# Kernel tuning notes

Hardware: AMD Instinct MI355X
Metric: run time of the kernel (lower is better)

## Reference

```python
import jax, jax.numpy as jnp
import numpy as np

NEG_INF = float('-inf')

def setup_inputs() -> dict:
    key = jax.random.key(0)
    k1, k2, k3, k4 = jax.random.split(key, 4)
    B, H, S, D = 2, 16, 2048, 64
    query = jax.random.normal(k1, (B, H, S, D), dtype=jnp.float32)
    k_ = jax.random.normal(k2, (B, H, S, D), dtype=jnp.float32)
    v_ = jax.random.normal(k3, (B, H, S, D), dtype=jnp.float32)
    attn_mask = jax.random.randint(k4, (B, S, S), 0, 2).astype(bool)
    # ensure diagonal is unmasked so every causal row has >=1 valid key
    diag = jnp.arange(S)
    attn_mask = attn_mask.at[:, diag, diag].set(True)
    return {"query": query, "key": k_, "value": v_, "attn_mask": attn_mask}

def reference(query, key, value, attn_mask):
    # query/key/value: [B, H, S, D]; attn_mask: [B, S, S] bool, True = keep
    B, H, S, D = query.shape
    scale = D ** (-0.5)
    scores = jnp.einsum('bhqd,bhkd->bhqk', query, key) * scale
    # custom mask (True = keep)
    scores = jnp.where(attn_mask[:, None, :, :], scores, NEG_INF)
    # causal mask: disallow j > i
    causal = jnp.triu(jnp.ones((S, S), dtype=bool), k=1)  # True above diagonal
    scores = jnp.where(causal[None, None, :, :], NEG_INF, scores)
    probs = jax.nn.softmax(scores, axis=-1)
    # dropout omitted (eval mode / deterministic reference)
    out = jnp.einsum('bhqk,bhkd->bhqd', probs, value)
    return out
```

## Files before the change

### kernel.cpp

```cpp
#include <hip/hip_runtime.h>
#include <hip/hip_bf16.h>

#define NS 2048
#define ND 64

typedef __attribute__((ext_vector_type(8))) short short8;
typedef __attribute__((ext_vector_type(4))) short short4v;
typedef __attribute__((ext_vector_type(4))) float f32x4;

static __device__ __forceinline__ short f2bf(float f) {
    union { __hip_bfloat16 h; short s; } u;
    u.h = __float2bfloat16(f);
    return u.s;
}
static __device__ __forceinline__ unsigned int pack2(float lo, float hi) {
    return (unsigned int)(unsigned short)f2bf(lo) |
           ((unsigned int)(unsigned short)f2bf(hi) << 16);
}
static __device__ __forceinline__ float exp2_fast(float x) {
    float r;
    asm("v_exp_f32 %0, %1" : "=v"(r) : "v"(x));
    return r;
}
static __device__ __forceinline__ unsigned int cvt_pk_bf16(float lo, float hi) {
    unsigned int w;
    asm("v_cvt_pk_bf16_f32 %0, %1, %2" : "=v"(w) : "v"(lo), "v"(hi));
    return w;
}

__global__ void detect_mask_kernel(const unsigned char* __restrict__ mask,
                                   int* __restrict__ flag) {
    const int i = threadIdx.x;
    unsigned int acc = 0;
    const uchar4* p = (const uchar4*)(mask + i * 64);
    #pragma unroll
    for (int j = 0; j < 16; ++j) {
        uchar4 v = p[j];
        acc |= (unsigned int)v.y | v.z | v.w;
    }
    const unsigned long long any = __ballot(acc != 0);
    if (i == 0) *flag = (any == 0ULL) ? 4 : 1;
}

__global__ void prep_all(const float* __restrict__ K,
                         const float* __restrict__ V,
                         const unsigned char* __restrict__ M,
                         const int* __restrict__ flag,
                         unsigned char* __restrict__ IMG,
                         unsigned int* __restrict__ Mbits) {
    if (blockIdx.x < 2048) {
        const int bid = blockIdx.x;
        const int bh = bid >> 6, T = bid & 63;
        const int i = threadIdx.x;
        __shared__ __align__(16) unsigned char img[8192];

        const int row = i >> 3;
        const int d0  = (i & 7) * 8;

        {
            const float* src = K + ((size_t)(bh * NS + T * 32 + row)) * ND + d0;
            float4 f0 = ((const float4*)src)[0];
            float4 f1 = ((const float4*)src)[1];
            const float f[8] = {f0.x, f0.y, f0.z, f0.w, f1.x, f1.y, f1.z, f1.w};
            const int n = row >> 4, cc = row & 15;
            #pragma unroll
            for (int jp = 0; jp < 4; ++jp) {
                const int d  = d0 + 2 * jp;
                const int ch = d >> 5, dd = d & 31;
                const int g  = (dd & 15) >> 2;
                const int jj = (dd >> 4) * 2 + ((dd >> 1) & 1);
                *(unsigned int*)(img + (n * 2 + ch) * 1024 + (g * 16 + cc) * 16 + jj * 4) =
                    pack2(f[2 * jp], f[2 * jp + 1]);
            }
        }
        {
            const int kv = row;
            const float* src = V + ((size_t)(bh * NS + T * 32 + kv)) * ND + d0;
            float4 f0 = ((const float4*)src)[0];
            float4 f1 = ((const float4*)src)[1];
            const float f[8] = {f0.x, f0.y, f0.z, f0.w, f1.x, f1.y, f1.z, f1.w};
            const int kl  = kv & ~1;
            const int q15 = kl & 15;
            const int g   = q15 >> 2;
            const int jj  = (kl >> 4) * 2 + ((q15 >> 1) & 1);
            const int half = (kv & 1) * 2;
            #pragma unroll
            for (int e = 0; e < 8; ++e) {
                const int d  = d0 + e;
                const int n4 = d >> 4, cv = d & 15;
                *(short*)(img + 4096 + n4 * 1024 + (g * 16 + cv) * 16 + jj * 4 + half) =
                    f2bf(f[e]);
            }
        }
        __syncthreads();
        uint4* dst = (uint4*)(IMG + ((size_t)bid << 13));
        const uint4* srcl = (const uint4*)img;
        dst[i * 2]     = srcl[i * 2];
        dst[i * 2 + 1] = srcl[i * 2 + 1];
    } else {
        const int id3 = (blockIdx.x - 2048) * 256 + threadIdx.x;
        const int tt = id3 & 63, q = (id3 >> 6) & 2047, b = id3 >> 17;
        const int ms = *flag;
        unsigned int w = 0;
        if (ms == 1) {
            const uint4* p = (const uint4*)(M + ((size_t)(b * NS + q)) * NS + tt * 32);
            uint4 A = p[0], B = p[1];
            const unsigned int u[8] = {A.x, A.y, A.z, A.w, B.x, B.y, B.z, B.w};
            #pragma unroll
            for (int i = 0; i < 8; ++i) {
                const unsigned int nib = (((u[i] & 0x01010101u) * 0x01020408u) >> 24) & 0xFu;
                w |= nib << (4 * i);
            }
        } else {
            const uint4* p = (const uint4*)(M + (((size_t)(b * NS + q)) * NS) * 4 + tt * 128);
            #pragma unroll
            for (int i = 0; i < 8; ++i) {
                uint4 A = p[i];
                w |= ((A.x & 1u) << (4 * i)) | ((A.y & 1u) << (4 * i + 1)) |
                     ((A.z & 1u) << (4 * i + 2)) | ((A.w & 1u) << (4 * i + 3));
            }
        }
        const int qrel = q - 32 * tt;
        if (qrel < 0) w = 0;
        else if (qrel < 31) w &= ((2u << qrel) - 1u);
        Mbits[((size_t)(b * 64 + (q >> 5)) * 64 + tt) * 32 + (q & 31)] = w;
    }
}

#define GLD(gsrc, ldst) __builtin_amdgcn_global_load_lds( \
    (const __attribute__((address_space(1))) unsigned int*)(gsrc), \
    (__attribute__((address_space(3))) unsigned int*)(ldst), 16, 0, 0)

__launch_bounds__(256, 4)
__global__ void attn_main(const float* __restrict__ Q,
                          const unsigned char* __restrict__ IMG,
                          const unsigned int* __restrict__ Mbits,
                          float* __restrict__ O) {
    const int idx = blockIdx.x;
    const int j   = (idx & 511) >> 5;
    const int bh  = idx & 31;
    const int qi  = (idx < 512) ? (31 - j) : j;
    const int b   = bh >> 4;

    const int tid  = threadIdx.x;
    const int wid  = tid >> 6;
    const int lane = tid & 63;
    const int g = lane >> 4;
    const int c = lane & 15;
    const int p = wid & 1;
    const int s = wid >> 1;

    const int q0w = qi * 64 + s * 32;

    const size_t bhoff = (size_t)bh * NS * ND;
    const float* Qb = Q + bhoff;
    float*       Ob = O + bhoff;
    const unsigned char* Tb = IMG + ((size_t)bh << 19);
    const unsigned int*  Mw = Mbits + ((size_t)(b * 64 + 2 * qi + s) << 11);

    __shared__ __align__(16) unsigned char smem[2][16384];

    const float QS = 0.18033688f;
    short8 aq[2][2];
    #pragma unroll
    for (int m = 0; m < 2; ++m) {
        const float* qrow = Qb + (size_t)(q0w + m * 16 + c) * ND;
        #pragma unroll
        for (int ch = 0; ch < 2; ++ch) {
            float4 x0 = *reinterpret_cast<const float4*>(qrow + ch * 32 + g * 4);
            float4 x1 = *reinterpret_cast<const float4*>(qrow + ch * 32 + 16 + g * 4);
            short8 fr;
            fr[0]=f2bf(x0.x*QS); fr[1]=f2bf(x0.y*QS); fr[2]=f2bf(x0.z*QS); fr[3]=f2bf(x0.w*QS);
            fr[4]=f2bf(x1.x*QS); fr[5]=f2bf(x1.y*QS); fr[6]=f2bf(x1.z*QS); fr[7]=f2bf(x1.w*QS);
            aq[m][ch] = fr;
        }
    }

    const short ov = (c == 0) ? (short)0x3F80 : (short)0;
    short8 onesf;
    #pragma unroll
    for (int e = 0; e < 8; ++e) onesf[e] = ov;

    f32x4 acc[2][4];
    f32x4 acc_l[2];
    #pragma unroll
    for (int m = 0; m < 2; ++m) {
        acc_l[m] = (f32x4){0.f, 0.f, 0.f, 0.f};
        #pragma unroll
        for (int n4 = 0; n4 < 4; ++n4) acc[m][n4] = (f32x4){0.f, 0.f, 0.f, 0.f};
    }

    const int NP   = qi + 1;
    const int tmax = 2 * qi + s;

#define STAGE(B, TP) do { \
    const unsigned char* gp_ = Tb + ((size_t)(2 * (TP)) << 13) + (wid << 10) + (lane << 4); \
    unsigned char* lb_ = &smem[B][wid << 10]; \
    GLD(gp_,         lb_); \
    GLD(gp_ +  4096, lb_ +  4096); \
    GLD(gp_ +  8192, lb_ +  8192); \
    GLD(gp_ + 12288, lb_ + 12288); \
} while (0)

    STAGE(0, 0);
    unsigned int mk0 = Mw[p * 32 + c];
    unsigned int mk1 = Mw[p * 32 + 16 + c];
    asm volatile("s_waitcnt vmcnt(0)" ::: "memory");
    __syncthreads();

    for (int tp = 0; tp < NP; ++tp) {
        const int cur = tp & 1;
        const int t = 2 * tp + p;
        const bool havenext = (tp + 1 < NP);
        unsigned int nk0 = 0, nk1 = 0;
        if (havenext) {
            STAGE(cur ^ 1, tp + 1);
            nk0 = Mw[(t + 2) * 32 + c];
            nk1 = Mw[(t + 2) * 32 + 16 + c];
        }

        if (t <= tmax) {
            const unsigned char* kb = smem[cur] + (p << 13);
            const unsigned char* vb = kb + 4096;

            short8 kf[4], av[4];
            #pragma unroll
            for (int k4 = 0; k4 < 4; ++k4)
                kf[k4] = *(const short8*)(kb + k4 * 1024 + (lane << 4));
            #pragma unroll
            for (int n4 = 0; n4 < 4; ++n4)
                av[n4] = *(const short8*)(vb + n4 * 1024 + (lane << 4));

            #pragma unroll
            for (int m = 0; m < 2; ++m) {
                f32x4 s0 = (f32x4){0.f, 0.f, 0.f, 0.f};
                f32x4 s1 = (f32x4){0.f, 0.f, 0.f, 0.f};
                s0 = __builtin_amdgcn_mfma_f32_16x16x32_bf16(kf[0], aq[m][0], s0, 0, 0, 0);
                s0 = __builtin_amdgcn_mfma_f32_16x16x32_bf16(kf[1], aq[m][1], s0, 0, 0, 0);
                s1 = __builtin_amdgcn_mfma_f32_16x16x32_bf16(kf[2], aq[m][0], s1, 0, 0, 0);
                s1 = __builtin_amdgcn_mfma_f32_16x16x32_bf16(kf[3], aq[m][1], s1, 0, 0, 0);

                const unsigned int mk = m ? mk1 : mk0;

                float pv[8];
                #pragma unroll
                for (int r = 0; r < 4; ++r) {
                    const unsigned int b0 = (mk >> (4 * g + r)) & 1u;
                    const unsigned int b1 = (mk >> (16 + 4 * g + r)) & 1u;
                    pv[r]     = exp2_fast(b0 ? s0[r] : -INFINITY);
                    pv[4 + r] = exp2_fast(b1 ? s1[r] : -INFINITY);
                }
                union { unsigned int u[4]; short8 v; } pfu;
                pfu.u[0] = cvt_pk_bf16(pv[0], pv[1]);
                pfu.u[1] = cvt_pk_bf16(pv[2], pv[3]);
                pfu.u[2] = cvt_pk_bf16(pv[4], pv[5]);
                pfu.u[3] = cvt_pk_bf16(pv[6], pv[7]);
                const short8 pf = pfu.v;

                #pragma unroll
                for (int n4 = 0; n4 < 4; ++n4)
                    acc[m][n4] = __builtin_amdgcn_mfma_f32_16x16x32_bf16(av[n4], pf, acc[m][n4], 0, 0, 0);
                acc_l[m] = __builtin_amdgcn_mfma_f32_16x16x32_bf16(onesf, pf, acc_l[m], 0, 0, 0);
            }
        }

        mk0 = nk0; mk1 = nk1;
        asm volatile("s_waitcnt vmcnt(0)" ::: "memory");
        __syncthreads();
    }

    float* MB = (float*)smem;
    __syncthreads();
    if (p == 1) {
        #pragma unroll
        for (int m = 0; m < 2; ++m) {
            #pragma unroll
            for (int n4 = 0; n4 < 4; ++n4)
                *(f32x4*)&MB[(((s * 2 + m) * 4 + n4) * 64 + lane) * 4] = acc[m][n4];
            *(f32x4*)&MB[4096 + ((s * 2 + m) * 64 + lane) * 4] = acc_l[m];
        }
    }
    __syncthreads();
    if (p == 0) {
        #pragma unroll
        for (int m = 0; m < 2; ++m) {
            #pragma unroll
            for (int n4 = 0; n4 < 4; ++n4) {
                f32x4 o = *(const f32x4*)&MB[(((s * 2 + m) * 4 + n4) * 64 + lane) * 4];
                acc[m][n4][0] += o[0]; acc[m][n4][1] += o[1];
                acc[m][n4][2] += o[2]; acc[m][n4][3] += o[3];
            }
            f32x4 ol = *(const f32x4*)&MB[4096 + ((s * 2 + m) * 64 + lane) * 4];
            acc_l[m][0] += ol[0];
        }
        #pragma unroll
        for (int m = 0; m < 2; ++m) {
            const int q = q0w + m * 16 + c;
            const float lsum = __shfl(acc_l[m][0], c);
            const float inv = (lsum > 0.f) ? (1.f / lsum) : 0.f;
            float* orow = Ob + (size_t)q * ND;
            #pragma unroll
            for (int n4 = 0; n4 < 4; ++n4) {
                float4 o;
                o.x = acc[m][n4][0] * inv;
                o.y = acc[m][n4][1] * inv;
                o.z = acc[m][n4][2] * inv;
                o.w = acc[m][n4][3] * inv;
                *(float4*)(orow + n4 * 16 + 4 * g) = o;
            }
        }
    }
#undef STAGE
}

__launch_bounds__(128, 2)
__global__ void attn_fwd_fb(const float* __restrict__ Q,
                            const float* __restrict__ K,
                            const float* __restrict__ V,
                            const unsigned char* __restrict__ M,
                            float* __restrict__ O,
                            const int* __restrict__ mstride_p) {
    const int ms  = *mstride_p;
    const int idx = blockIdx.x;
    const int qi  = 31 - (idx >> 5);
    const int bh  = idx & 31;
    const int b   = bh >> 4;

    const int tid  = threadIdx.x;
    const int wid  = tid >> 6;
    const int lane = tid & 63;
    const int g = lane >> 4;
    const int c = lane & 15;

    const int q0w = qi * 64 + wid * 32;

    const size_t bhoff = (size_t)bh * NS * ND;
    const float* Qb = Q + bhoff;
    const float* Kb = K + bhoff;
    const float* Vb = V + bhoff;
    float*       Ob = O + bhoff;
    const unsigned char* Mb = M + (size_t)b * NS * NS * (size_t)ms;

    __shared__ __align__(16) unsigned char smem[2][8192];

    short8 aq[2][2];
    #pragma unroll
    for (int m = 0; m < 2; ++m) {
        const float* qrow = Qb + (size_t)(q0w + m * 16 + c) * ND;
        #pragma unroll
        for (int ch = 0; ch < 2; ++ch) {
            float4 x0 = *reinterpret_cast<const float4*>(qrow + ch * 32 + g * 4);
            float4 x1 = *reinterpret_cast<const float4*>(qrow + ch * 32 + 16 + g * 4);
            short8 fr;
            fr[0]=f2bf(x0.x); fr[1]=f2bf(x0.y); fr[2]=f2bf(x0.z); fr[3]=f2bf(x0.w);
            fr[4]=f2bf(x1.x); fr[5]=f2bf(x1.y); fr[6]=f2bf(x1.z); fr[7]=f2bf(x1.w);
            aq[m][ch] = fr;
        }
    }

    f32x4 acc[2][4];
    float m_run[2], l_run[2];
    #pragma unroll
    for (int m = 0; m < 2; ++m) {
        m_run[m] = -INFINITY; l_run[m] = 0.f;
        #pragma unroll
        for (int n4 = 0; n4 < 4; ++n4) acc[m][n4] = (f32x4){0.f, 0.f, 0.f, 0.f};
    }

    const int NT = 2 * qi + 2;

    const int krow = tid >> 2;
    const int kcb  = (tid & 3) * 16;
    const int ksw  = (krow & 7) << 4;
    const int vkp  = tid >> 3;
    const int vdb  = tid & 7;
    const int vg   = (vkp >> 1) & 3;
    const int vep  = (vkp & 1) + 2 * (vkp >> 3);
    const float* kbase = Kb + (size_t)krow * ND + kcb;
    const float* vbase = Vb + (size_t)(2 * vkp) * ND + vdb * 8;

    float4 kin0, kin1, kin2, kin3, vin0, vin1, vin2, vin3;

#define STAGE_LOAD(T) do { \
    const float* kp_ = kbase + (size_t)(T) * 32 * ND; \
    kin0 = *(const float4*)(kp_);      kin1 = *(const float4*)(kp_ + 4); \
    kin2 = *(const float4*)(kp_ + 8);  kin3 = *(const float4*)(kp_ + 12); \
    const float* vp_ = vbase + (size_t)(T) * 32 * ND; \
    vin0 = *(const float4*)(vp_);      vin1 = *(const float4*)(vp_ + 4); \
    vin2 = *(const float4*)(vp_ + ND); vin3 = *(const float4*)(vp_ + ND + 4); \
} while (0)

#define STAGE_WRITE(BUF) do { \
    unsigned char* kb_ = smem[BUF]; \
    short8 w0, w1; \
    w0[0]=f2bf(kin0.x); w0[1]=f2bf(kin0.y); w0[2]=f2bf(kin0.z); w0[3]=f2bf(kin0.w); \
    w0[4]=f2bf(kin1.x); w0[5]=f2bf(kin1.y); w0[6]=f2bf(kin1.z); w0[7]=f2bf(kin1.w); \
    w1[0]=f2bf(kin2.x); w1[1]=f2bf(kin2.y); w1[2]=f2bf(kin2.z); w1[3]=f2bf(kin2.w); \
    w1[4]=f2bf(kin3.x); w1[5]=f2bf(kin3.y); w1[6]=f2bf(kin3.z); w1[7]=f2bf(kin3.w); \
    *(short8*)(kb_ + krow * 128 + ((kcb * 2) ^ ksw))      = w0; \
    *(short8*)(kb_ + krow * 128 + ((kcb * 2 + 16) ^ ksw)) = w1; \
    unsigned char* vb_ = smem[BUF] + 4096; \
    const float lo_[8] = {vin0.x, vin0.y, vin0.z, vin0.w, vin1.x, vin1.y, vin1.z, vin1.w}; \
    const float hi_[8] = {vin2.x, vin2.y, vin2.z, vin2.w, vin3.x, vin3.y, vin3.z, vin3.w}; \
    _Pragma("unroll") \
    for (int j_ = 0; j_ < 8; ++j_) { \
        const int d_ = vdb * 8 + j_; \
        const int n4_ = d_ >> 4; \
        const int cc_ = d_ & 15; \
        const int aw_ = ((n4_ * 4 + vep) * 64 + ((vg * 16 + cc_) ^ ((vep << 3) | n4_))) * 4; \
        *(unsigned int*)(vb_ + aw_) = pack2(lo_[j_], hi_[j_]); \
    } \
} while (0)

    STAGE_LOAD(0);
    STAGE_WRITE(0);
    __syncthreads();

    const float SC = 0.125f;

    for (int t = 0; t < NT; ++t) {
        const int cur = t & 1;
        const bool havenext = (t + 1 < NT);
        if (havenext) STAGE_LOAD(t + 1);

        const unsigned char* kb = smem[cur];
        const int sw = (c & 7) << 4;
        short8 kf[2][2];
        #pragma unroll
        for (int n = 0; n < 2; ++n) {
            const int row = n * 16 + c;
            #pragma unroll
            for (int ch = 0; ch < 2; ++ch) {
                short4v lo = *(const short4v*)(kb + row * 128 + ((ch * 64 + g * 8) ^ sw));
                short4v hi = *(const short4v*)(kb + row * 128 + ((ch * 64 + g * 8 + 32) ^ sw));
                short8 fr;
                fr[0]=lo[0]; fr[1]=lo[1]; fr[2]=lo[2]; fr[3]=lo[3];
                fr[4]=hi[0]; fr[5]=hi[1]; fr[6]=hi[2]; fr[7]=hi[3];
                kf[n][ch] = fr;
            }
        }
        const unsigned char* vbuf = smem[cur] + 4096;
        short8 av[4];
        #pragma unroll
        for (int n4 = 0; n4 < 4; ++n4) {
            short8 fr;
            #pragma unroll
            for (int ep = 0; ep < 4; ++ep) {
                unsigned int w = *(const unsigned int*)
                    (vbuf + (((n4 * 4 + ep) * 64 + (lane ^ ((ep << 3) | n4))) * 4));
                fr[2 * ep]     = (short)(w & 0xffff);
                fr[2 * ep + 1] = (short)(w >> 16);
            }
            av[n4] = fr;
        }

        const int kv0 = t * 32;
        #pragma unroll
        for (int m = 0; m < 2; ++m) {
            const int q = q0w + m * 16 + c;

            f32x4 s[2];
            #pragma unroll
            for (int n = 0; n < 2; ++n) {
                f32x4 z = {0.f, 0.f, 0.f, 0.f};
                z = __builtin_amdgcn_mfma_f32_16x16x32_bf16(kf[n][0], aq[m][0], z, 0, 0, 0);
                z = __builtin_amdgcn_mfma_f32_16x16x32_bf16(kf[n][1], aq[m][1], z, 0, 0, 0);
                s[n] = z;
            }

            unsigned int mk0, mk1;
            if (ms == 1) {
                mk0 = *(const unsigned int*)(Mb + (size_t)q * NS + kv0 + 4 * g);
                mk1 = *(const unsigned int*)(Mb + (size_t)q * NS + kv0 + 16 + 4 * g);
            } else {
                const uint4 a4 = *(const uint4*)(Mb + ((size_t)q * NS + kv0 + 4 * g) * 4);
                const uint4 b4 = *(const uint4*)(Mb + ((size_t)q * NS + kv0 + 16 + 4 * g) * 4);
                mk0 = (a4.x?1u:0u) | (a4.y?0x100u:0u) | (a4.z?0x10000u:0u) | (a4.w?0x1000000u:0u);
                mk1 = (b4.x?1u:0u) | (b4.y?0x100u:0u) | (b4.z?0x10000u:0u) | (b4.w?0x1000000u:0u);
            }

            float mx = -INFINITY;
            #pragma unroll
            for (int n = 0; n < 2; ++n) {
                const unsigned int mk = n ? mk1 : mk0;
                #pragma unroll
                for (int r = 0; r < 4; ++r) {
                    const int kv = kv0 + n * 16 + 4 * g + r;
                    const bool keep = (((mk >> (8 * r)) & 0xffu) != 0u) && (kv <= q);
                    const float val = keep ? s[n][r] * SC : -INFINITY;
                    s[n][r] = val;
                    mx = fmaxf(mx, val);
                }
            }
            mx = fmaxf(mx, __shfl_xor(mx, 16));
            mx = fmaxf(mx, __shfl_xor(mx, 32));

            const float m_new = fmaxf(m_run[m], mx);
            const float alpha = (m_run[m] == -INFINITY) ? 0.f : __expf(m_run[m] - m_new);
            m_run[m] = m_new;
            const float msafe = (m_new == -INFINITY) ? 0.f : m_new;

            float sum = 0.f;
            short8 pf;
            #pragma unroll
            for (int n = 0; n < 2; ++n)
                #pragma unroll
                for (int r = 0; r < 4; ++r) {
                    const float pvv = __expf(s[n][r] - msafe);
                    sum += pvv;
                    pf[n * 4 + r] = f2bf(pvv);
                }
            sum += __shfl_xor(sum, 16);
            sum += __shfl_xor(sum, 32);
            l_run[m] = l_run[m] * alpha + sum;

            #pragma unroll
            for (int n4 = 0; n4 < 4; ++n4) {
                f32x4 o = acc[m][n4];
                o[0] *= alpha; o[1] *= alpha; o[2] *= alpha; o[3] *= alpha;
                o = __builtin_amdgcn_mfma_f32_16x16x32_bf16(av[n4], pf, o, 0, 0, 0);
                acc[m][n4] = o;
            }
        }

        if (havenext) STAGE_WRITE(cur ^ 1);
        __syncthreads();
    }

    #pragma unroll
    for (int m = 0; m < 2; ++m) {
        const int q = q0w + m * 16 + c;
        const float inv = (l_run[m] > 0.f) ? (1.f / l_run[m]) : 0.f;
        float* orow = Ob + (size_t)q * ND;
        #pragma unroll
        for (int n4 = 0; n4 < 4; ++n4) {
            float4 o;
            o.x = acc[m][n4][0] * inv;
            o.y = acc[m][n4][1] * inv;
            o.z = acc[m][n4][2] * inv;
            o.w = acc[m][n4][3] * inv;
            *(float4*)(orow + n4 * 16 + 4 * g) = o;
        }
    }
#undef STAGE_LOAD
#undef STAGE_WRITE
}

extern "C" void kernel_launch(void* const* d_in, const int* in_sizes, int n_in,
                              void* d_out, int out_size, void* d_ws, size_t ws_size,
                              hipStream_t stream) {
    const float* Q = (const float*)d_in[0];
    const float* K = (const float*)d_in[1];
    const float* V = (const float*)d_in[2];
    const unsigned char* M = (const unsigned char*)d_in[3];
    float* O = (float*)d_out;

    unsigned char* ws = (unsigned char*)d_ws;
    int* flag = (int*)ws;
    const size_t IMG_SZ  = (size_t)2048 * 8192;
    const size_t BITS_SZ = (size_t)2 * 64 * 64 * 32 * 4;
    const size_t NEED = 1024 + IMG_SZ + BITS_SZ;

    hipLaunchKernelGGL(detect_mask_kernel, dim3(1), dim3(64), 0, stream, M, flag);

    if (ws_size >= NEED) {
        unsigned char* IMG  = ws + 1024;
        unsigned int* Mbits = (unsigned int*)(ws + 1024 + IMG_SZ);
        hipLaunchKernelGGL(prep_all, dim3(3072), dim3(256), 0, stream,
                           K, V, M, flag, IMG, Mbits);
        hipLaunchKernelGGL(attn_main, dim3(1024), dim3(256), 0, stream,
                           Q, IMG, Mbits, O);
    } else {
        hipLaunchKernelGGL(attn_fwd_fb, dim3(1024), dim3(128), 0, stream,
                           Q, K, V, M, O, flag);
    }
}
```

Measured before the change: 54.28 us.

## Load K/V tiles directly to registers and fold mask detection into prep kernel

The main attention kernel stops staging K/V tile images through LDS with global_load_lds and barriers. Each wave now loads its own tile fragments straight into registers, double-buffered in software with two register sets, and the per-iteration __syncthreads is gone. The separate mask-format detection launch is removed: every mask-packing block recomputes the flag from the first mask bytes and shares it through LDS. The launch-bounds occupancy hint is dropped, which trades more register pressure and less shared-memory reuse for fewer barriers and one less kernel launch.

```diff
diff --git a/kernel.cpp b/kernel.cpp
--- a/kernel.cpp
+++ b/kernel.cpp
@@ -45,7 +45,6 @@
 __global__ void prep_all(const float* __restrict__ K,
                          const float* __restrict__ V,
                          const unsigned char* __restrict__ M,
-                         const int* __restrict__ flag,
                          unsigned char* __restrict__ IMG,
                          unsigned int* __restrict__ Mbits) {
     if (blockIdx.x < 2048) {
@@ -98,9 +97,26 @@
         dst[i * 2]     = srcl[i * 2];
         dst[i * 2 + 1] = srcl[i * 2 + 1];
     } else {
+        __shared__ int msh;
+        {
+            unsigned int accv = 0;
+            if (threadIdx.x < 64) {
+                const uint4* p4 = (const uint4*)(M + threadIdx.x * 64);
+                #pragma unroll
+                for (int jj = 0; jj < 4; ++jj) {
+                    uint4 v = p4[jj];
+                    accv |= (v.x & 0xFFFFFF00u) | (v.y & 0xFFFFFF00u) |
+                            (v.z & 0xFFFFFF00u) | (v.w & 0xFFFFFF00u);
+                }
+            }
+            const unsigned long long any = __ballot(accv != 0);
+            if (threadIdx.x == 0) msh = (any == 0ULL) ? 4 : 1;
+        }
+        __syncthreads();
+        const int ms = msh;
+
         const int id3 = (blockIdx.x - 2048) * 256 + threadIdx.x;
         const int tt = id3 & 63, q = (id3 >> 6) & 2047, b = id3 >> 17;
-        const int ms = *flag;
         unsigned int w = 0;
         if (ms == 1) {
             const uint4* p = (const uint4*)(M + ((size_t)(b * NS + q)) * NS + tt * 32);
@@ -127,11 +143,7 @@
     }
 }
 
-#define GLD(gsrc, ldst) __builtin_amdgcn_global_load_lds( \
-    (const __attribute__((address_space(1))) unsigned int*)(gsrc), \
-    (__attribute__((address_space(3))) unsigned int*)(ldst), 16, 0, 0)
-
-__launch_bounds__(256, 4)
+__launch_bounds__(256)
 __global__ void attn_main(const float* __restrict__ Q,
                           const unsigned char* __restrict__ IMG,
                           const unsigned int* __restrict__ Mbits,
@@ -158,7 +170,7 @@
     const unsigned char* Tb = IMG + ((size_t)bh << 19);
     const unsigned int*  Mw = Mbits + ((size_t)(b * 64 + 2 * qi + s) << 11);
 
-    __shared__ __align__(16) unsigned char smem[2][16384];
+    __shared__ __align__(16) float MB[5120];
 
     const float QS = 0.18033688f;
     short8 aq[2][2];
@@ -190,87 +202,68 @@
         for (int n4 = 0; n4 < 4; ++n4) acc[m][n4] = (f32x4){0.f, 0.f, 0.f, 0.f};
     }
 
-    const int NP   = qi + 1;
     const int tmax = 2 * qi + s;
 
-#define STAGE(B, TP) do { \
-    const unsigned char* gp_ = Tb + ((size_t)(2 * (TP)) << 13) + (wid << 10) + (lane << 4); \
-    unsigned char* lb_ = &smem[B][wid << 10]; \
-    GLD(gp_,         lb_); \
-    GLD(gp_ +  4096, lb_ +  4096); \
-    GLD(gp_ +  8192, lb_ +  8192); \
-    GLD(gp_ + 12288, lb_ + 12288); \
+#define LOADT(T, KF, AV, MK0, MK1) do { \
+    const short8* tp_ = (const short8*)(Tb + ((size_t)(T) << 13) + (lane << 4)); \
+    KF[0] = tp_[0];   KF[1] = tp_[64];  KF[2] = tp_[128]; KF[3] = tp_[192]; \
+    AV[0] = tp_[256]; AV[1] = tp_[320]; AV[2] = tp_[384]; AV[3] = tp_[448]; \
+    MK0 = Mw[(T) * 32 + c]; \
+    MK1 = Mw[(T) * 32 + 16 + c]; \
 } while (0)
 
-    STAGE(0, 0);
-    unsigned int mk0 = Mw[p * 32 + c];
-    unsigned int mk1 = Mw[p * 32 + 16 + c];
-    asm volatile("s_waitcnt vmcnt(0)" ::: "memory");
-    __syncthreads();
-
-    for (int tp = 0; tp < NP; ++tp) {
-        const int cur = tp & 1;
-        const int t = 2 * tp + p;
-        const bool havenext = (tp + 1 < NP);
-        unsigned int nk0 = 0, nk1 = 0;
-        if (havenext) {
-            STAGE(cur ^ 1, tp + 1);
-            nk0 = Mw[(t + 2) * 32 + c];
-            nk1 = Mw[(t + 2) * 32 + 16 + c];
-        }
-
+#define COMPUTE(KF, AV, MK0, MK1) do { \
+    _Pragma("unroll") \
+    for (int m = 0; m < 2; ++m) { \
+        f32x4 s0 = (f32x4){0.f, 0.f, 0.f, 0.f}; \
+        f32x4 s1 = (f32x4){0.f, 0.f, 0.f, 0.f}; \
+        s0 = __builtin_amdgcn_mfma_f32_16x16x32_bf16(KF[0], aq[m][0], s0, 0, 0, 0); \
+        s0 = __builtin_amdgcn_mfma_f32_16x16x32_bf16(KF[1], aq[m][1], s0, 0, 0, 0); \
+        s1 = __builtin_amdgcn_mfma_f32_16x16x32_bf16(KF[2], aq[m][0], s1, 0, 0, 0); \
+        s1 = __builtin_amdgcn_mfma_f32_16x16x32_bf16(KF[3], aq[m][1], s1, 0, 0, 0); \
+        const unsigned int mk = m ? (MK1) : (MK0); \
+        float pv[8]; \
+        _Pragma("unroll") \
+        for (int r = 0; r < 4; ++r) { \
+            const unsigned int b0 = (mk >> (4 * g + r)) & 1u; \
+            const unsigned int b1 = (mk >> (16 + 4 * g + r)) & 1u; \
+            pv[r]     = exp2_fast(b0 ? s0[r] : -INFINITY); \
+            pv[4 + r] = exp2_fast(b1 ? s1[r] : -INFINITY); \
+        } \
+        union { unsigned int u[4]; short8 v; } pfu_; \
+        pfu_.u[0] = cvt_pk_bf16(pv[0], pv[1]); \
+        pfu_.u[1] = cvt_pk_bf16(pv[2], pv[3]); \
+        pfu_.u[2] = cvt_pk_bf16(pv[4], pv[5]); \
+        pfu_.u[3] = cvt_pk_bf16(pv[6], pv[7]); \
+        const short8 pf = pfu_.v; \
+        _Pragma("unroll") \
+        for (int n4 = 0; n4 < 4; ++n4) \
+            acc[m][n4] = __builtin_amdgcn_mfma_f32_16x16x32_bf16(AV[n4], pf, acc[m][n4], 0, 0, 0); \
+        acc_l[m] = __builtin_amdgcn_mfma_f32_16x16x32_bf16(onesf, pf, acc_l[m], 0, 0, 0); \
+    } \
+} while (0)
+
+    {
+        short8 kfA[4], avA[4], kfB[4], avB[4];
+        unsigned int a0 = 0, a1 = 0, b0m = 0, b1m = 0;
+        int t = p;
         if (t <= tmax) {
-            const unsigned char* kb = smem[cur] + (p << 13);
-            const unsigned char* vb = kb + 4096;
-
-            short8 kf[4], av[4];
-            #pragma unroll
-            for (int k4 = 0; k4 < 4; ++k4)
-                kf[k4] = *(const short8*)(kb + k4 * 1024 + (lane << 4));
-            #pragma unroll
-            for (int n4 = 0; n4 < 4; ++n4)
-                av[n4] = *(const short8*)(vb + n4 * 1024 + (lane << 4));
-
-            #pragma unroll
-            for (int m = 0; m < 2; ++m) {
-                f32x4 s0 = (f32x4){0.f, 0.f, 0.f, 0.f};
-                f32x4 s1 = (f32x4){0.f, 0.f, 0.f, 0.f};
-                s0 = __builtin_amdgcn_mfma_f32_16x16x32_bf16(kf[0], aq[m][0], s0, 0, 0, 0);
-                s0 = __builtin_amdgcn_mfma_f32_16x16x32_bf16(kf[1], aq[m][1], s0, 0, 0, 0);
-                s1 = __builtin_amdgcn_mfma_f32_16x16x32_bf16(kf[2], aq[m][0], s1, 0, 0, 0);
-                s1 = __builtin_amdgcn_mfma_f32_16x16x32_bf16(kf[3], aq[m][1], s1, 0, 0, 0);
-
-                const unsigned int mk = m ? mk1 : mk0;
-
-                float pv[8];
-                #pragma unroll
-                for (int r = 0; r < 4; ++r) {
-                    const unsigned int b0 = (mk >> (4 * g + r)) & 1u;
-                    const unsigned int b1 = (mk >> (16 + 4 * g + r)) & 1u;
-                    pv[r]     = exp2_fast(b0 ? s0[r] : -INFINITY);
-                    pv[4 + r] = exp2_fast(b1 ? s1[r] : -INFINITY);
-                }
-                union { unsigned int u[4]; short8 v; } pfu;
-                pfu.u[0] = cvt_pk_bf16(pv[0], pv[1]);
-                pfu.u[1] = cvt_pk_bf16(pv[2], pv[3]);
-                pfu.u[2] = cvt_pk_bf16(pv[4], pv[5]);
-                pfu.u[3] = cvt_pk_bf16(pv[6], pv[7]);
-                const short8 pf = pfu.v;
-
-                #pragma unroll
-                for (int n4 = 0; n4 < 4; ++n4)
-                    acc[m][n4] = __builtin_amdgcn_mfma_f32_16x16x32_bf16(av[n4], pf, acc[m][n4], 0, 0, 0);
-                acc_l[m] = __builtin_amdgcn_mfma_f32_16x16x32_bf16(onesf, pf, acc_l[m], 0, 0, 0);
-            }
-        }
-
-        mk0 = nk0; mk1 = nk1;
-        asm volatile("s_waitcnt vmcnt(0)" ::: "memory");
-        __syncthreads();
-    }
-
-    float* MB = (float*)smem;
-    __syncthreads();
+            LOADT(t, kfA, avA, a0, a1);
+            for (;;) {
+                const int tn = t + 2;
+                if (tn <= tmax) LOADT(tn, kfB, avB, b0m, b1m);
+                COMPUTE(kfA, avA, a0, a1);
+                t = tn;
+                if (t > tmax) break;
+                const int tn2 = t + 2;
+                if (tn2 <= tmax) LOADT(tn2, kfA, avA, a0, a1);
+                COMPUTE(kfB, avB, b0m, b1m);
+                t = tn2;
+                if (t > tmax) break;
+            }
+        }
+    }
+
     if (p == 1) {
         #pragma unroll
         for (int m = 0; m < 2; ++m) {
@@ -310,7 +303,8 @@
             }
         }
     }
-#undef STAGE
+#undef LOADT
+#undef COMPUTE
 }
 
 __launch_bounds__(128, 2)
@@ -556,21 +550,20 @@
     float* O = (float*)d_out;
 
     unsigned char* ws = (unsigned char*)d_ws;
-    int* flag = (int*)ws;
     const size_t IMG_SZ  = (size_t)2048 * 8192;
     const size_t BITS_SZ = (size_t)2 * 64 * 64 * 32 * 4;
     const size_t NEED = 1024 + IMG_SZ + BITS_SZ;
-
-    hipLaunchKernelGGL(detect_mask_kernel, dim3(1), dim3(64), 0, stream, M, flag);
 
     if (ws_size >= NEED) {
         unsigned char* IMG  = ws + 1024;
         unsigned int* Mbits = (unsigned int*)(ws + 1024 + IMG_SZ);
         hipLaunchKernelGGL(prep_all, dim3(3072), dim3(256), 0, stream,
-                           K, V, M, flag, IMG, Mbits);
+                           K, V, M, IMG, Mbits);
         hipLaunchKernelGGL(attn_main, dim3(1024), dim3(256), 0, stream,
                            Q, IMG, Mbits, O);
     } else {
+        int* flag = (int*)ws;
+        hipLaunchKernelGGL(detect_mask_kernel, dim3(1), dim3(64), 0, stream, M, flag);
         hipLaunchKernelGGL(attn_fwd_fb, dim3(1024), dim3(128), 0, stream,
                            Q, K, V, M, O, flag);
     }
```

New measurement: 61.56 us. 1.13x slower.
